# Kernel tuning notes

Hardware: AMD Instinct MI355X
Metric: run time of the kernel (lower is better)

Reference implementation:

```python
import jax, jax.numpy as jnp
import numpy as np
from jax import lax

# Reconstruction of MVC (manifold/log-domain voxel conv):
#   log_forward : v = Conv3d(Log_M(x), w) in the log domain, base point M = per-voxel
#                 geometric mean over input channels (Log_M(x) = log x - log M on R+).
#   exp_forward : out = Exp_M(v) = M * exp(v).
# The custom autograd (grad_x + grad_M) corresponds to input gradients flowing through
# both the log-domain conv and the base point M.

B, CIN, COUT, K = 2, 16, 16, 3
D = H = W = 96


def setup_inputs() -> dict:
    key = jax.random.key(0)
    k1, k2 = jax.random.split(key)
    # strictly positive voxel values (fODF coefficients) so log is well-defined
    x = jax.random.uniform(k1, (B, CIN, D, H, W), dtype=jnp.float32,
                           minval=0.05, maxval=1.0)
    weights = jax.random.uniform(k2, (COUT, K, K, K, CIN), dtype=jnp.float32)
    return {"x": x, "weights": weights}


def reference(x, weights):
    logx = jnp.log(x)                                   # [B, Cin, D, H, W]
    logM = jnp.mean(logx, axis=1, keepdims=True)        # per-voxel base point, [B,1,D,H,W]
    # log_forward: 3D conv of tangent vectors (log x - log M)
    w = jnp.transpose(weights, (0, 4, 1, 2, 3))         # [Cout, Cin, K, K, K] (OIDHW)
    conv = lax.conv_general_dilated(
        logx, w, window_strides=(1, 1, 1), padding='SAME',
        dimension_numbers=('NCDHW', 'OIDHW', 'NCDHW'))  # [B, Cout, D, H, W]
    wsum = jnp.sum(weights, axis=(1, 2, 3, 4))          # [Cout], accounts for -logM term
    out_log = conv - wsum[None, :, None, None, None] * logM
    # exp_forward: Exp_M(v) = M * exp(v) = exp(logM + v)
    return jnp.exp(logM + out_log)
```

## Files before the change

### kernel.cpp

```cpp
#include <hip/hip_runtime.h>


#define VOX  884736
#define SLX  98
#define ROWS (SLX * 16)
#define SROWS 4
#define SSs  (SROWS * ROWS)
#define SSb  (SSs * 2)
#define NSL  4
#define TY   2
#define ZC   12

typedef __attribute__((ext_vector_type(8))) short short8;
typedef __attribute__((ext_vector_type(4))) float f32x4;

__device__ __forceinline__ unsigned short f2bf_rne(float f) {
    unsigned u = __float_as_uint(f);
    u += 0x7fff + ((u >> 16) & 1);
    return (unsigned short)(u >> 16);
}
__device__ __forceinline__ float bf2f(short s) {
    return __uint_as_float(((unsigned)(unsigned short)s) << 16);
}

__global__ void mvc_reorg(const float* __restrict__ w,
                          short* __restrict__ w3,
                          float* __restrict__ wadj) {
    int i = blockIdx.x * 256 + threadIdx.x;
    if (i < 16 * 448) {
        int n = i / 448, k = i % 448;
        int p = k >> 5, q = (k >> 3) & 3, j = k & 7;
        int qhi = q >> 1, ci = (q & 1) * 8 + j;
        int tap;
        bool valid = true;
        if (p < 9)        tap = (p / 3) * 9 + (p % 3) * 3 + qhi;
        else if (p < 12)  tap = (p - 9) * 9 + qhi * 3 + 2;
        else if (p == 12) tap = qhi * 9 + 8;
        else { tap = 26; valid = (qhi == 0); }
        float v = valid ? w[n * 432 + tap * 16 + ci] : 0.0f;
        w3[i] = (short)f2bf_rne(v);
    }
    if (i < 16) {
        const float* pw = w + i * 432;
        float s = 0.0f;
        for (int t = 0; t < 432; ++t) s += pw[t];
        wadj[i] = 1.0f - s;
    }
}

__global__ void __launch_bounds__(256)
mvc_log(const float* __restrict__ x, short* __restrict__ lx) {
    const int id = blockIdx.x;
    const int b = id / 3456;
    const size_t v = (size_t)(id - b * 3456) * 256 + threadIdx.x;
    const float* xb = x + (size_t)b * 16 * VOX + v;
    unsigned rbuf[8];
    #pragma unroll
    for (int c = 0; c < 8; ++c) {
        unsigned lo = f2bf_rne(__logf(xb[(size_t)(2 * c) * VOX]));
        unsigned hi = f2bf_rne(__logf(xb[(size_t)(2 * c + 1) * VOX]));
        rbuf[c] = lo | (hi << 16);
    }
    unsigned* dst = (unsigned*)(lx + ((size_t)b * VOX + v) * 16);
    *(uint4*)dst       = make_uint4(rbuf[0], rbuf[1], rbuf[2], rbuf[3]);
    *(uint4*)(dst + 4) = make_uint4(rbuf[4], rbuf[5], rbuf[6], rbuf[7]);
}

__global__ void __launch_bounds__(256, 3)
mvc_conv(const short* __restrict__ lx,
         const short* __restrict__ w3,
         const float* __restrict__ wadj,
         float* __restrict__ out) {
    __shared__ __align__(16) short tile[NSL * SSs + 512];

    const int tid  = threadIdx.x;
    const int lane = tid & 63;
    const int wv   = tid >> 6;
    const int mn   = lane & 15;
    const int q    = lane >> 4;
    const int qlo  = q & 1;
    const int qhi  = q >> 1;

    int id  = blockIdx.x;
    int xcd = id & 7, g = id >> 3;
    int yt  = xcd * 6 + g % 6;
    int rr  = g / 6;
    int zch = rr % 8, b = rr / 8;
    const int y0 = yt * TY;
    const int z0 = zch * ZC;

    const short* lxb = lx + (size_t)b * VOX * 16;
    float* ob = out + (size_t)b * 16 * VOX;

    short8 bfr[14];
    #pragma unroll
    for (int p = 0; p < 14; ++p)
        bfr[p] = *(const short8*)(w3 + mn * 448 + p * 32 + q * 8);
    const float4 wv4 = *(const float4*)(wadj + 4 * q);
    const float wa[4] = {wv4.x, wv4.y, wv4.z, wv4.w};
    const short oc = qhi ? (short)0x3D80 : (short)0;
    const short8 aones = {oc, oc, oc, oc, oc, oc, oc, oc};

    auto stage = [&](int zp) {
        const int sl = zp & 3;
        const int gy = y0 - 1 + wv;
        const bool vr = (unsigned)gy < 96u;
        const int gyc = vr ? gy : 0;
        const short* gsrc = lxb + (size_t)(zp * 9216 + gyc * 96) * 16 + lane * 8;
        short* lrow = tile + sl * SSs + (wv * SLX + 1) * 16;
        short* ltr  = tile + NSL * SSs;
        #pragma unroll
        for (int k = 0; k < 3; ++k) {
            short* dst = vr ? (lrow + k * 512) : ltr;
            __builtin_amdgcn_global_load_lds(
                (const __attribute__((address_space(1))) unsigned int*)(const void*)(gsrc + k * 512),
                (__attribute__((address_space(3))) unsigned int*)(void*)dst,
                16, 0, 0);
        }
    };
    auto zero_slice = [&](int sl) {
        #pragma unroll
        for (int i = 0; i < 4; ++i) {
            int c = tid + i * 256;
            if (c < 784)
                *(f32x4*)((char*)tile + sl * SSb + c * 16) = (f32x4){0.f, 0.f, 0.f, 0.f};
        }
    };

    if (tid < 64) {
        int s = tid >> 4, rest = tid & 15;
        int row = rest >> 2, side = (rest >> 1) & 1, half = tid & 1;
        *(f32x4*)((char*)tile + s * SSb + (row * SLX + side * 97) * 32 + half * 16)
            = (f32x4){0.f, 0.f, 0.f, 0.f};
    }
    if (yt == 0 || yt == 47) {
        int row = (yt == 0) ? 0 : 3;
        #pragma unroll
        for (int s = 0; s < 4; ++s)
            if (tid < 196)
                *(f32x4*)((char*)tile + s * SSb + row * 3136 + tid * 16)
                    = (f32x4){0.f, 0.f, 0.f, 0.f};
    }
    if (z0 == 0) zero_slice(3); else stage(z0 - 1);
    stage(z0);
    stage(z0 + 1);

    #pragma unroll 1
    for (int zi = 0; zi < ZC; ++zi) {
        const int z = z0 + zi;
        asm volatile("s_waitcnt vmcnt(0)" ::: "memory");
        __syncthreads();
        if (zi < ZC - 1) {
            const int zp = z + 2;
            if (zp < 96) stage(zp);
            else         zero_slice(zp & 3);
        }
        __builtin_amdgcn_sched_barrier(0);

        const int B0 = ((z + 3) & 3) * SSs;
        const int B1 = (z & 3) * SSs;
        const int B2 = ((z + 1) & 3) * SSs;
        const int r  = wv >> 1;
        const int xh = wv & 1;
        const int Lb = mn * 16 + qlo * 8 + r * ROWS + qhi * 16;

        #pragma unroll
        for (int jj = 0; jj < 3; ++jj) {
            const int j = xh * 3 + jj;
            const short* vA0 = tile + (Lb + j * 256 + B0);
            const short* vA1 = tile + (Lb + j * 256 + B1);
            const short* vA2 = tile + (Lb + j * 256 + B2);
            const short* vB0 = vA0 + 32 + qhi * 1552;
            const short* vB1 = vA1 + 32 + qhi * 1552;
            const short* vB2 = vA2 + 32 + qhi * 1552;
            const short* vD  = vB2 + (3136 - qhi * 1584);
            const short* vC  = vD - B2 + (qhi ? B1 : B0);

            f32x4 acc = {0.f, 0.f, 0.f, 0.f};
            acc = __builtin_amdgcn_mfma_f32_16x16x32_bf16(bfr[0],  *(const short8*)(vA0),        acc, 0, 0, 0);
            acc = __builtin_amdgcn_mfma_f32_16x16x32_bf16(bfr[1],  *(const short8*)(vA0 + 1568), acc, 0, 0, 0);
            acc = __builtin_amdgcn_mfma_f32_16x16x32_bf16(bfr[2],  *(const short8*)(vA0 + 3136), acc, 0, 0, 0);
            acc = __builtin_amdgcn_mfma_f32_16x16x32_bf16(bfr[3],  *(const short8*)(vA1),        acc, 0, 0, 0);
            acc = __builtin_amdgcn_mfma_f32_16x16x32_bf16(bfr[4],  *(const short8*)(vA1 + 1568), acc, 0, 0, 0);
            acc = __builtin_amdgcn_mfma_f32_16x16x32_bf16(bfr[5],  *(const short8*)(vA1 + 3136), acc, 0, 0, 0);
            acc = __builtin_amdgcn_mfma_f32_16x16x32_bf16(bfr[6],  *(const short8*)(vA2),        acc, 0, 0, 0);
            acc = __builtin_amdgcn_mfma_f32_16x16x32_bf16(bfr[7],  *(const short8*)(vA2 + 1568), acc, 0, 0, 0);
            acc = __builtin_amdgcn_mfma_f32_16x16x32_bf16(bfr[8],  *(const short8*)(vA2 + 3136), acc, 0, 0, 0);
            acc = __builtin_amdgcn_mfma_f32_16x16x32_bf16(bfr[9],  *(const short8*)(vB0),        acc, 0, 0, 0);
            acc = __builtin_amdgcn_mfma_f32_16x16x32_bf16(bfr[10], *(const short8*)(vB1),        acc, 0, 0, 0);
            acc = __builtin_amdgcn_mfma_f32_16x16x32_bf16(bfr[11], *(const short8*)(vB2),        acc, 0, 0, 0);
            acc = __builtin_amdgcn_mfma_f32_16x16x32_bf16(bfr[12], *(const short8*)(vC),         acc, 0, 0, 0);
            acc = __builtin_amdgcn_mfma_f32_16x16x32_bf16(bfr[13], *(const short8*)(vD),         acc, 0, 0, 0);

            f32x4 am = __builtin_amdgcn_mfma_f32_16x16x32_bf16(
                aones, *(const short8*)(vA1 + 1568), (f32x4){0.f, 0.f, 0.f, 0.f}, 0, 0, 0);
            const float lm = am[0];

            float* op = ob + (size_t)(4 * q) * VOX
                      + (((size_t)z * 96 + (y0 + r)) * 96 + j * 16 + mn);
            #pragma unroll
            for (int t = 0; t < 4; ++t) {
                float e = fminf(fmaf(wa[t], lm, acc[t]), 88.0f);
                op[(size_t)t * VOX] = __expf(e);
            }
        }
    }
}

#define FSLY  6
#define FROWS (SLX * 16)
#define FSS   (FSLY * FROWS)
#define FTY   4
#define FZC   6

__global__ void __launch_bounds__(256, 2)
mvc_main(const float* __restrict__ x,
         const short* __restrict__ w3,
         const float* __restrict__ wadj,
         float* __restrict__ out) {
    __shared__ __align__(16) short tile[3 * FSS];
    __shared__ float logMt[FTY * 96];

    const int tid  = threadIdx.x;
    const int lane = tid & 63;
    const int wv   = tid >> 6;
    const int mn   = lane & 15;
    const int q    = lane >> 4;
    const int qlo  = q & 1;
    const int qhi  = q >> 1;

    int id  = blockIdx.x;
    int xcd = id & 7, g = id >> 3;
    int yt  = xcd * 3 + g % 3;
    int rr  = g / 3;
    int zch = rr & 15, b = rr >> 4;
    const int y0 = yt * FTY;
    const int z0 = zch * FZC;

    const float* xb = x + (size_t)b * 16 * VOX;
    float* ob = out + (size_t)b * 16 * VOX;

    short8 bfr[14];
    #pragma unroll
    for (int p = 0; p < 14; ++p)
        bfr[p] = *(const short8*)(w3 + mn * 448 + p * 32 + q * 8);
    const float4 wv4 = *(const float4*)(wadj + 4 * q);
    const float wa[4] = {wv4.x, wv4.y, wv4.z, wv4.w};

    if (tid < 288) {
        int d = tid & 7, vv = tid >> 3;
        int bu = vv / 12, rv = vv % 12;
        int row = rv >> 1, side = rv & 1;
        ((unsigned*)tile)[bu * (FSS / 2) + (row * SLX + side * 97) * 8 + d] = 0u;
    }

    float2 h[5][4];

    auto load_plane = [&](int zp) {
        bool zin = (unsigned)zp < 96u;
        #pragma unroll
        for (int it = 0; it < 5; ++it) {
            if (it == 4 && tid >= 128) break;
            int slot = tid + it * 256;
            int cq = slot & 3;
            int t  = slot >> 2;
            int xp = t % 48;
            int y  = t / 48;
            int gy = y0 + y - 1;
            bool inb = zin && ((unsigned)gy < 96u);
            const float* p0 = xb + (size_t)(4 * cq) * VOX
                            + ((zp * 96 + gy) * 96 + 2 * xp);
            h[it][0] = inb ? *(const float2*)(p0)            : make_float2(1.f, 1.f);
            h[it][1] = inb ? *(const float2*)(p0 + VOX)      : make_float2(1.f, 1.f);
            h[it][2] = inb ? *(const float2*)(p0 + 2 * VOX)  : make_float2(1.f, 1.f);
            h[it][3] = inb ? *(const float2*)(p0 + 3 * VOX)  : make_float2(1.f, 1.f);
        }
    };
    auto write_plane = [&](int zp) {
        short* sb = tile + ((zp + 3) % 3) * FSS;
        #pragma unroll
        for (int it = 0; it < 5; ++it) {
            if (it == 4 && tid >= 128) break;
            int slot = tid + it * 256;
            int cq = slot & 3;
            int t  = slot >> 2;
            int xp = t % 48;
            int y  = t / 48;
            unsigned a0 = f2bf_rne(__logf(h[it][0].x)), a1 = f2bf_rne(__logf(h[it][1].x));
            unsigned a2 = f2bf_rne(__logf(h[it][2].x)), a3 = f2bf_rne(__logf(h[it][3].x));
            unsigned c0 = f2bf_rne(__logf(h[it][0].y)), c1 = f2bf_rne(__logf(h[it][1].y));
            unsigned c2 = f2bf_rne(__logf(h[it][2].y)), c3 = f2bf_rne(__logf(h[it][3].y));
            unsigned* dst = (unsigned*)(sb + (y * SLX + 1 + 2 * xp) * 16 + 4 * cq);
            *(uint2*)(dst)     = make_uint2(a0 | (a1 << 16), a2 | (a3 << 16));
            *(uint2*)(dst + 8) = make_uint2(c0 | (c1 << 16), c2 | (c3 << 16));
        }
    };
    auto do_logM = [&](int z) {
        const short* cb = tile + (z % 3) * FSS;
        #pragma unroll
        for (int it = 0; it < 2; ++it) {
            if (it == 1 && tid >= 128) break;
            int v = tid + it * 256;
            int xx = v % 96, yy = v / 96;
            const short* p = cb + ((yy + 1) * SLX + (xx + 1)) * 16;
            short8 h0 = *(const short8*)p;
            short8 h1 = *(const short8*)(p + 8);
            float s = 0.f;
            #pragma unroll
            for (int c = 0; c < 8; ++c) s += bf2f(h0[c]) + bf2f(h1[c]);
            logMt[v] = s * 0.0625f;
        }
    };

    load_plane(z0 - 1); write_plane(z0 - 1);
    load_plane(z0);     write_plane(z0);
    load_plane(z0 + 1); write_plane(z0 + 1);
    __syncthreads();

    for (int zi = 0; zi < FZC; ++zi) {
        const int z = z0 + zi;
        const bool st = (zi < FZC - 1);
        if (st) load_plane(z + 2);
        do_logM(z);
        __syncthreads();

        const int B0 = ((z + 2) % 3) * FSS;
        const int B1 = (z % 3) * FSS;
        const int B2 = ((z + 1) % 3) * FSS;
        const int Lb = mn * 16 + qlo * 8 + wv * FROWS + qhi * 16;

        #pragma unroll
        for (int j = 0; j < 6; ++j) {
            const short* vA0 = tile + (Lb + j * 256 + B0);
            const short* vA1 = tile + (Lb + j * 256 + B1);
            const short* vA2 = tile + (Lb + j * 256 + B2);
            const short* vB0 = vA0 + 32 + qhi * 1552;
            const short* vB1 = vA1 + 32 + qhi * 1552;
            const short* vB2 = vA2 + 32 + qhi * 1552;
            const short* vD  = vB2 + (3136 - qhi * 1584);
            const short* vC  = vD - B2 + (qhi ? B1 : B0);

            f32x4 acc = {0.f, 0.f, 0.f, 0.f};
            acc = __builtin_amdgcn_mfma_f32_16x16x32_bf16(bfr[0],  *(const short8*)(vA0),        acc, 0, 0, 0);
            acc = __builtin_amdgcn_mfma_f32_16x16x32_bf16(bfr[1],  *(const short8*)(vA0 + 1568), acc, 0, 0, 0);
            acc = __builtin_amdgcn_mfma_f32_16x16x32_bf16(bfr[2],  *(const short8*)(vA0 + 3136), acc, 0, 0, 0);
            acc = __builtin_amdgcn_mfma_f32_16x16x32_bf16(bfr[3],  *(const short8*)(vA1),        acc, 0, 0, 0);
            acc = __builtin_amdgcn_mfma_f32_16x16x32_bf16(bfr[4],  *(const short8*)(vA1 + 1568), acc, 0, 0, 0);
            acc = __builtin_amdgcn_mfma_f32_16x16x32_bf16(bfr[5],  *(const short8*)(vA1 + 3136), acc, 0, 0, 0);
            acc = __builtin_amdgcn_mfma_f32_16x16x32_bf16(bfr[6],  *(const short8*)(vA2),        acc, 0, 0, 0);
            acc = __builtin_amdgcn_mfma_f32_16x16x32_bf16(bfr[7],  *(const short8*)(vA2 + 1568), acc, 0, 0, 0);
            acc = __builtin_amdgcn_mfma_f32_16x16x32_bf16(bfr[8],  *(const short8*)(vA2 + 3136), acc, 0, 0, 0);
            acc = __builtin_amdgcn_mfma_f32_16x16x32_bf16(bfr[9],  *(const short8*)(vB0),        acc, 0, 0, 0);
            acc = __builtin_amdgcn_mfma_f32_16x16x32_bf16(bfr[10], *(const short8*)(vB1),        acc, 0, 0, 0);
            acc = __builtin_amdgcn_mfma_f32_16x16x32_bf16(bfr[11], *(const short8*)(vB2),        acc, 0, 0, 0);
            acc = __builtin_amdgcn_mfma_f32_16x16x32_bf16(bfr[12], *(const short8*)(vC),         acc, 0, 0, 0);
            acc = __builtin_amdgcn_mfma_f32_16x16x32_bf16(bfr[13], *(const short8*)(vD),         acc, 0, 0, 0);

            float lm = logMt[wv * 96 + j * 16 + mn];
            float* op = ob + (size_t)(4 * q) * VOX
                      + (((size_t)z * 96 + (y0 + wv)) * 96 + j * 16 + mn);
            #pragma unroll
            for (int t = 0; t < 4; ++t) {
                float e = fminf(fmaf(wa[t], lm, acc[t]), 88.0f);
                op[(size_t)t * VOX] = __expf(e);
            }
        }
        __syncthreads();
        if (st) write_plane(z + 2);
    }
}

extern "C" void kernel_launch(void* const* d_in, const int* in_sizes, int n_in,
                              void* d_out, int out_size, void* d_ws, size_t ws_size,
                              hipStream_t stream) {
    const float* x = (const float*)d_in[0];
    const float* w = (const float*)d_in[1];
    float* out  = (float*)d_out;
    short* w3   = (short*)d_ws;
    float* wadj = (float*)((char*)d_ws + 14336);
    short* lgx  = (short*)((char*)d_ws + 16384);

    const size_t lx_full = (size_t)2 * VOX * 16 * 2;
    const size_t lx_half = (size_t)VOX * 16 * 2;

    hipLaunchKernelGGL(mvc_reorg, dim3(28), dim3(256), 0, stream, w, w3, wadj);

    if (ws_size >= 16384 + lx_full) {
        hipLaunchKernelGGL(mvc_log,  dim3(6912), dim3(256), 0, stream, x, lgx);
        hipLaunchKernelGGL(mvc_conv, dim3(768),  dim3(256), 0, stream, lgx, w3, wadj, out);
    } else if (ws_size >= 16384 + lx_half) {
        for (int b = 0; b < 2; ++b) {
            hipLaunchKernelGGL(mvc_log,  dim3(3456), dim3(256), 0, stream,
                               x + (size_t)b * 16 * VOX, lgx);
            hipLaunchKernelGGL(mvc_conv, dim3(384),  dim3(256), 0, stream,
                               lgx, w3, wadj, out + (size_t)b * 16 * VOX);
        }
    } else {
        hipLaunchKernelGGL(mvc_main, dim3(768), dim3(256), 0, stream, x, w3, wadj, out);
    }
}
```

Measured before the change: 242.7 us.

## Fuse weight reorg into log kernel and relax conv loop barrier waits

The weight-reorganisation kernel is merged into the log-conversion kernel as 28 extra blocks, which removes one launch from the main path. In the conv kernel, the per-iteration full vmcnt(0) wait plus barrier at the top of the loop is replaced by a partial vmcnt(12) wait and barrier at the end of each iteration. This lets the prefetch of the next slice stay in flight while compute proceeds. The partial wait count is tied to the number of loads issued by stage, so a wrong count could cause LDS races.

```diff
diff --git a/kernel.cpp b/kernel.cpp
--- a/kernel.cpp
+++ b/kernel.cpp
@@ -23,10 +23,9 @@
     return __uint_as_float(((unsigned)(unsigned short)s) << 16);
 }
 
-__global__ void mvc_reorg(const float* __restrict__ w,
-                          short* __restrict__ w3,
-                          float* __restrict__ wadj) {
-    int i = blockIdx.x * 256 + threadIdx.x;
+__device__ __forceinline__ void reorg_body(int i, const float* __restrict__ w,
+                                           short* __restrict__ w3,
+                                           float* __restrict__ wadj) {
     if (i < 16 * 448) {
         int n = i / 448, k = i % 448;
         int p = k >> 5, q = (k >> 3) & 3, j = k & 7;
@@ -48,6 +47,36 @@
     }
 }
 
+__global__ void mvc_reorg(const float* __restrict__ w,
+                          short* __restrict__ w3,
+                          float* __restrict__ wadj) {
+    reorg_body(blockIdx.x * 256 + threadIdx.x, w, w3, wadj);
+}
+
+__global__ void __launch_bounds__(256)
+mvc_logr(const float* __restrict__ x, short* __restrict__ lx,
+         const float* __restrict__ w, short* __restrict__ w3,
+         float* __restrict__ wadj) {
+    const int id = blockIdx.x;
+    if (id >= 6912) {
+        reorg_body((id - 6912) * 256 + threadIdx.x, w, w3, wadj);
+        return;
+    }
+    const int b = id / 3456;
+    const size_t v = (size_t)(id - b * 3456) * 256 + threadIdx.x;
+    const float* xb = x + (size_t)b * 16 * VOX + v;
+    unsigned rbuf[8];
+    #pragma unroll
+    for (int c = 0; c < 8; ++c) {
+        unsigned lo = f2bf_rne(__logf(xb[(size_t)(2 * c) * VOX]));
+        unsigned hi = f2bf_rne(__logf(xb[(size_t)(2 * c + 1) * VOX]));
+        rbuf[c] = lo | (hi << 16);
+    }
+    unsigned* dst = (unsigned*)(lx + ((size_t)b * VOX + v) * 16);
+    *(uint4*)dst       = make_uint4(rbuf[0], rbuf[1], rbuf[2], rbuf[3]);
+    *(uint4*)(dst + 4) = make_uint4(rbuf[4], rbuf[5], rbuf[6], rbuf[7]);
+}
+
 __global__ void __launch_bounds__(256)
 mvc_log(const float* __restrict__ x, short* __restrict__ lx) {
     const int id = blockIdx.x;
@@ -144,12 +173,11 @@
     if (z0 == 0) zero_slice(3); else stage(z0 - 1);
     stage(z0);
     stage(z0 + 1);
+    __syncthreads();
 
     #pragma unroll 1
     for (int zi = 0; zi < ZC; ++zi) {
         const int z = z0 + zi;
-        asm volatile("s_waitcnt vmcnt(0)" ::: "memory");
-        __syncthreads();
         if (zi < ZC - 1) {
             const int zp = z + 2;
             if (zp < 96) stage(zp);
@@ -204,6 +232,12 @@
                 op[(size_t)t * VOX] = __expf(e);
             }
         }
+
+        if (zi < ZC - 1) {
+            asm volatile("s_waitcnt vmcnt(12) lgkmcnt(0)" ::: "memory");
+            __builtin_amdgcn_s_barrier();
+            __builtin_amdgcn_sched_barrier(0);
+        }
     }
 }
 
@@ -383,12 +417,13 @@
     const size_t lx_full = (size_t)2 * VOX * 16 * 2;
     const size_t lx_half = (size_t)VOX * 16 * 2;
 
-    hipLaunchKernelGGL(mvc_reorg, dim3(28), dim3(256), 0, stream, w, w3, wadj);
-
     if (ws_size >= 16384 + lx_full) {
-        hipLaunchKernelGGL(mvc_log,  dim3(6912), dim3(256), 0, stream, x, lgx);
-        hipLaunchKernelGGL(mvc_conv, dim3(768),  dim3(256), 0, stream, lgx, w3, wadj, out);
+        hipLaunchKernelGGL(mvc_logr, dim3(6940), dim3(256), 0, stream,
+                           x, lgx, w, w3, wadj);
+        hipLaunchKernelGGL(mvc_conv, dim3(768),  dim3(256), 0, stream,
+                           lgx, w3, wadj, out);
     } else if (ws_size >= 16384 + lx_half) {
+        hipLaunchKernelGGL(mvc_reorg, dim3(28), dim3(256), 0, stream, w, w3, wadj);
         for (int b = 0; b < 2; ++b) {
             hipLaunchKernelGGL(mvc_log,  dim3(3456), dim3(256), 0, stream,
                                x + (size_t)b * 16 * VOX, lgx);
@@ -396,6 +431,7 @@
                                lgx, w3, wadj, out + (size_t)b * 16 * VOX);
         }
     } else {
+        hipLaunchKernelGGL(mvc_reorg, dim3(28), dim3(256), 0, stream, w, w3, wadj);
         hipLaunchKernelGGL(mvc_main, dim3(768), dim3(256), 0, stream, x, w3, wadj, out);
     }
 }
```

Result: faster. 237.4 us (-2.2%).
